# Performance work log

Measured on AMD Instinct MI355X. Metric: run time of the kernel, lower is better.

The kernel has to match this reference:

```python
import jax, jax.numpy as jnp
import numpy as np

B, S, F, H = 8, 2048, 512, 4
W = 32            # local window size
DH = F // H       # head dim
EPS = 1e-5


def layer_norm(x, w, b):
    mu = jnp.mean(x, axis=-1, keepdims=True)
    var = jnp.var(x, axis=-1, keepdims=True)
    return (x - mu) * jax.lax.rsqrt(var + EPS) * w + b


def mha(x, w_in, b_in, w_out, b_out):
    # x: [..., L, F]; torch nn.MultiheadAttention self-attention (dropout inactive / eval)
    qkv = x @ w_in.T + b_in                      # [..., L, 3F]
    q, k, v = jnp.split(qkv, 3, axis=-1)
    lead = x.shape[:-2]
    L = x.shape[-2]

    def heads(t):  # [..., L, F] -> [..., H, L, DH]
        return jnp.swapaxes(t.reshape(*lead, L, H, DH), -3, -2)

    q, k, v = heads(q), heads(k), heads(v)
    scores = jnp.einsum('...hld,...hmd->...hlm', q, k) / np.sqrt(DH)
    p = jax.nn.softmax(scores, axis=-1)
    o = jnp.einsum('...hlm,...hmd->...hld', p, v)  # [..., H, L, DH]
    o = jnp.swapaxes(o, -3, -2).reshape(*lead, L, F)
    return o @ w_out.T + b_out


def setup_inputs() -> dict:
    key = jax.random.key(0)
    ks = jax.random.split(key, 16)
    s = 0.02
    p = lambda k, shape: jax.random.normal(k, shape, dtype=jnp.float32) * s
    return {
        'x': jax.random.normal(ks[0], (B, S, F), dtype=jnp.float32),
        'l_in_w': p(ks[1], (3 * F, F)), 'l_in_b': p(ks[2], (3 * F,)),
        'l_out_w': p(ks[3], (F, F)),   'l_out_b': p(ks[4], (F,)),
        'g_in_w': p(ks[5], (3 * F, F)), 'g_in_b': p(ks[6], (3 * F,)),
        'g_out_w': p(ks[7], (F, F)),   'g_out_b': p(ks[8], (F,)),
        'n1_w': jnp.ones((F,)), 'n1_b': jnp.zeros((F,)),
        'n2_w': jnp.ones((F,)), 'n2_b': jnp.zeros((F,)),
        'gate_w': p(ks[9], (F, 2 * F)), 'gate_b': p(ks[10], (F,)),
        'gln_w': jnp.ones((F,)), 'gln_b': jnp.zeros((F,)),
    }


def reference(x, l_in_w, l_in_b, l_out_w, l_out_b,
              g_in_w, g_in_b, g_out_w, g_out_b,
              n1_w, n1_b, n2_w, n2_b,
              gate_w, gate_b, gln_w, gln_b):
    # local branch: block-diagonal (windowed) self-attention, all windows batched
    xw = x.reshape(B, S // W, W, F)
    local = mha(xw, l_in_w, l_in_b, l_out_w, l_out_b).reshape(B, S, F)
    local = layer_norm(x + local, n1_w, n1_b)
    # global branch: full self-attention
    glob = mha(x, g_in_w, g_in_b, g_out_w, g_out_b)
    glob = layer_norm(x + glob, n2_w, n2_b)
    # learned gate fusion
    gi = jnp.concatenate([local, glob], axis=-1)
    gate = jax.nn.sigmoid(layer_norm(gi @ gate_w.T + gate_b, gln_w, gln_b))
    return gate * local + (1.0 - gate) * glob
```

## Files before the change

### kernel.cpp

```cpp
#include <hip/hip_runtime.h>
#include <stdint.h>

#define BB 8
#define SS 2048
#define FF 512
#define HH 4
#define TOK (BB * SS)

typedef unsigned short u16;
typedef short short8 __attribute__((ext_vector_type(8)));
typedef float f32x4 __attribute__((ext_vector_type(4)));
typedef float f32x16 __attribute__((ext_vector_type(16)));

static __device__ __forceinline__ u16 f2bf(float f) {
  uint32_t u = __builtin_bit_cast(uint32_t, f);
  u = (u + 0x7fffu + ((u >> 16) & 1u)) >> 16;
  return (u16)u;
}

static __device__ __forceinline__ void cp16(void* lds, const void* g) {
  __builtin_amdgcn_global_load_lds(
      (const __attribute__((address_space(1))) void*)g,
      (__attribute__((address_space(3))) void*)lds, 16, 0, 0);
}

__global__ __launch_bounds__(256) void castk(const float* __restrict__ s,
                                             u16* __restrict__ d, int n) {
  const int i = (blockIdx.x * 256 + threadIdx.x) * 8;
  if (i >= n) return;
  float4 a = *(const float4*)(s + i);
  float4 b = *(const float4*)(s + i + 4);
  short8 o;
  o[0] = (short)f2bf(a.x); o[1] = (short)f2bf(a.y);
  o[2] = (short)f2bf(a.z); o[3] = (short)f2bf(a.w);
  o[4] = (short)f2bf(b.x); o[5] = (short)f2bf(b.y);
  o[6] = (short)f2bf(b.z); o[7] = (short)f2bf(b.w);
  *(short8*)(d + i) = o;
}

__global__ __launch_bounds__(256) void gemm_bt(
    const u16* __restrict__ A, const u16* __restrict__ B,
    const float* __restrict__ bias, float* __restrict__ Cf,
    u16* __restrict__ Cb, int M, int N, int K) {
  const int m0 = blockIdx.x << 7;
  const int n0 = blockIdx.y << 7;
  __shared__ u16 As[128 * 64];
  __shared__ u16 Bs[128 * 64];
  const int tid = threadIdx.x;
  const int wave = tid >> 6, lane = tid & 63;
  const int wr = wave >> 1, wc = wave & 1;

  f32x4 acc[4][4];
#pragma unroll
  for (int i = 0; i < 4; ++i)
#pragma unroll
    for (int j = 0; j < 4; ++j)
#pragma unroll
      for (int e = 0; e < 4; ++e) acc[i][j][e] = 0.f;

  for (int k0 = 0; k0 < K; k0 += 64) {
#pragma unroll
    for (int i = 0; i < 4; ++i) {
      const int base = (i * 4 + wave) << 10;
      const int lb = base + (lane << 4);
      const int r = lb >> 7;
      const int s = ((lb >> 4) & 7) ^ (r & 7);
      cp16((char*)As + base, A + (size_t)(m0 + r) * K + k0 + s * 8);
      cp16((char*)Bs + base, B + (size_t)(n0 + r) * K + k0 + s * 8);
    }
    __syncthreads();
#pragma unroll
    for (int kk = 0; kk < 2; ++kk) {
      short8 af[4], bfr[4];
#pragma unroll
      for (int mi = 0; mi < 4; ++mi) {
        const int r = wr * 64 + mi * 16 + (lane & 15);
        const int p = (kk * 4 + (lane >> 4)) ^ (r & 7);
        af[mi] = *(const short8*)(As + r * 64 + p * 8);
      }
#pragma unroll
      for (int ni = 0; ni < 4; ++ni) {
        const int r = wc * 64 + ni * 16 + (lane & 15);
        const int p = (kk * 4 + (lane >> 4)) ^ (r & 7);
        bfr[ni] = *(const short8*)(Bs + r * 64 + p * 8);
      }
#pragma unroll
      for (int mi = 0; mi < 4; ++mi)
#pragma unroll
        for (int ni = 0; ni < 4; ++ni)
          acc[mi][ni] = __builtin_amdgcn_mfma_f32_16x16x32_bf16(
              af[mi], bfr[ni], acc[mi][ni], 0, 0, 0);
    }
    __syncthreads();
  }
  const int rv = (lane >> 4) << 2;
  const int cn = lane & 15;
#pragma unroll
  for (int mi = 0; mi < 4; ++mi)
#pragma unroll
    for (int ni = 0; ni < 4; ++ni) {
      const int gn = n0 + wc * 64 + ni * 16 + cn;
      const float bv = bias ? bias[gn] : 0.f;
#pragma unroll
      for (int v = 0; v < 4; ++v) {
        const int gm = m0 + wr * 64 + mi * 16 + rv + v;
        const size_t off = (size_t)gm * N + gn;
        const float val = acc[mi][ni][v] + bv;
        if (Cf) Cf[off] = val;
        if (Cb) Cb[off] = f2bf(val);
      }
    }
}

__global__ __launch_bounds__(256) void transpose_v(
    const u16* __restrict__ qkv, u16* __restrict__ vt) {
  const int bh = blockIdx.x, st = blockIdx.y, dt = blockIdx.z;
  const int b = bh >> 2, h = bh & 3;
  __shared__ u16 t[64][72];
  const int r = threadIdx.x >> 3;
  const int c8 = (threadIdx.x & 7) * 8;
#pragma unroll
  for (int ph = 0; ph < 2; ++ph) {
    const int srow = ph * 32 + r;
    const u16* src = qkv + (size_t)(b * SS + st * 64 + srow) * 1536 + 1024 +
                     h * 128 + dt * 64 + c8;
    *(short8*)&t[srow][c8] = *(const short8*)src;
  }
  __syncthreads();
#pragma unroll
  for (int ph = 0; ph < 2; ++ph) {
    const int drow = ph * 32 + r;
    short8 o;
#pragma unroll
    for (int j = 0; j < 8; ++j) o[j] = (short)t[c8 + j][drow];
    *(short8*)(vt + ((size_t)bh * 128 + dt * 64 + drow) * SS + st * 64 + c8) = o;
  }
}

__global__ __launch_bounds__(256) void attn_local(
    const u16* __restrict__ qkv, const u16* __restrict__ vt,
    u16* __restrict__ ao) {
  const int wave = threadIdx.x >> 6, lane = threadIdx.x & 63;
  const int u = blockIdx.x * 4 + wave;
  const int b = u >> 8, w = (u >> 2) & 63, h = u & 3;
  const int q = lane & 31, half = lane >> 5;
  __shared__ u16 P[4][32][40];

  const size_t qbase = (size_t)(b * SS + w * 32 + q) * 1536 + h * 128;
  short8 qf[8];
#pragma unroll
  for (int d8 = 0; d8 < 8; ++d8)
    qf[d8] = *(const short8*)(qkv + qbase + d8 * 16 + half * 8);

  f32x16 s;
#pragma unroll
  for (int e = 0; e < 16; ++e) s[e] = 0.f;
  const size_t kbase = qbase + 512;
#pragma unroll
  for (int d8 = 0; d8 < 8; ++d8) {
    short8 kf = *(const short8*)(qkv + kbase + d8 * 16 + half * 8);
    s = __builtin_amdgcn_mfma_f32_32x32x16_bf16(kf, qf[d8], s, 0, 0, 0);
  }
  const float c1 = 0.12752725f;
  float m = -3e38f, t[16];
#pragma unroll
  for (int e = 0; e < 16; ++e) { t[e] = s[e] * c1; m = fmaxf(m, t[e]); }
  m = fmaxf(m, __shfl_xor(m, 32));
  float l = 0.f, p[16];
#pragma unroll
  for (int e = 0; e < 16; ++e) { p[e] = exp2f(t[e] - m); l += p[e]; }
  l += __shfl_xor(l, 32);
#pragma unroll
  for (int rr = 0; rr < 8; ++rr) {
    const int r0 = rr * 2;
    const int k0 = (r0 & 3) + 8 * (r0 >> 2) + 4 * half;
    uint32_t pk = (uint32_t)f2bf(p[r0]) | ((uint32_t)f2bf(p[r0 + 1]) << 16);
    *(uint32_t*)&P[wave][q][k0] = pk;
  }
  __syncthreads();
  f32x16 o[4];
#pragma unroll
  for (int nt = 0; nt < 4; ++nt)
#pragma unroll
    for (int e = 0; e < 16; ++e) o[nt][e] = 0.f;
  const size_t vbase = ((size_t)(b * 4 + h) * 128) * SS + w * 32;
#pragma unroll
  for (int ks = 0; ks < 2; ++ks) {
    short8 pa = *(const short8*)&P[wave][q][ks * 16 + half * 8];
#pragma unroll
    for (int nt = 0; nt < 4; ++nt) {
      short8 vb = *(const short8*)(vt + vbase + (size_t)(nt * 32 + q) * SS +
                                   ks * 16 + half * 8);
      o[nt] = __builtin_amdgcn_mfma_f32_32x32x16_bf16(pa, vb, o[nt], 0, 0, 0);
    }
  }
  const float rl = 1.f / l;
  const size_t ob = (size_t)(b * SS + w * 32) * FF + h * 128;
#pragma unroll
  for (int e = 0; e < 16; ++e) {
    const int qr = (e & 3) + 8 * (e >> 2) + 4 * half;
    const float rf = __shfl(rl, qr);
#pragma unroll
    for (int nt = 0; nt < 4; ++nt)
      ao[ob + (size_t)qr * FF + nt * 32 + q] = f2bf(o[nt][e] * rf);
  }
}

__global__ __launch_bounds__(256) void attn_global(
    const u16* __restrict__ qkv, const u16* __restrict__ vt,
    u16* __restrict__ ao) {
  const int lb = (blockIdx.x & 7) * 64 + (blockIdx.x >> 3);
  const int bh = lb >> 4, qt = lb & 15;
  const int b = bh >> 2, h = bh & 3;
  const int wave = threadIdx.x >> 6, lane = threadIdx.x & 63;
  const int q = lane & 31, half = lane >> 5;

  __shared__ u16 Ks[64 * 128];
  __shared__ u16 Vs[128 * 64];
  __shared__ u16 P[4][32][72];

  short8 qf[8];
  const size_t qb = (size_t)(b * SS + qt * 128 + wave * 32 + q) * 1536 + h * 128;
#pragma unroll
  for (int d8 = 0; d8 < 8; ++d8)
    qf[d8] = *(const short8*)(qkv + qb + d8 * 16 + half * 8);

  f32x16 o[4];
#pragma unroll
  for (int nt = 0; nt < 4; ++nt)
#pragma unroll
    for (int e = 0; e < 16; ++e) o[nt][e] = 0.f;
  float m = -3e38f, lsum = 0.f;
  const float c1 = 0.12752725f;

  const size_t kbase = (size_t)b * SS * 1536 + 512 + h * 128;
  const size_t vbase = (size_t)bh * 128 * SS;

  auto STAGE = [&](int kt) {
#pragma unroll
    for (int i = 0; i < 4; ++i) {
      const int base = (i * 4 + wave) << 10;
      const int lbk = base + (lane << 4);
      {
        const int r = lbk >> 8;
        const int sl = ((lbk >> 4) & 15) ^ (r & 7);
        cp16((char*)Ks + base,
             qkv + kbase + (size_t)(kt * 64 + r) * 1536 + sl * 8);
      }
      {
        const int d = lbk >> 7;
        const int sl = ((lbk >> 4) & 7) ^ (d & 7);
        cp16((char*)Vs + base, vt + vbase + (size_t)d * SS + kt * 64 + sl * 8);
      }
    }
  };
  STAGE(0);
  for (int kt = 0; kt < 32; ++kt) {
    __syncthreads();
    f32x16 sa[2];
#pragma unroll
    for (int mt = 0; mt < 2; ++mt)
#pragma unroll
      for (int e = 0; e < 16; ++e) sa[mt][e] = 0.f;
#pragma unroll
    for (int mt = 0; mt < 2; ++mt) {
      const int kr = mt * 32 + q;
#pragma unroll
      for (int d8 = 0; d8 < 8; ++d8) {
        const int ps = (d8 * 2 + half) ^ (kr & 7);
        short8 kf = *(const short8*)(Ks + kr * 128 + ps * 8);
        sa[mt] = __builtin_amdgcn_mfma_f32_32x32x16_bf16(kf, qf[d8], sa[mt], 0, 0, 0);
      }
    }
    float tv[32];
    float mn = m;
#pragma unroll
    for (int e = 0; e < 16; ++e) { tv[e] = sa[0][e] * c1; tv[16 + e] = sa[1][e] * c1; }
#pragma unroll
    for (int e = 0; e < 32; ++e) mn = fmaxf(mn, tv[e]);
    mn = fmaxf(mn, __shfl_xor(mn, 32));
    const float corr = exp2f(m - mn);
    m = mn;
    float la = 0.f;
#pragma unroll
    for (int e = 0; e < 32; ++e) { tv[e] = exp2f(tv[e] - mn); la += tv[e]; }
    la += __shfl_xor(la, 32);
    lsum = lsum * corr + la;
#pragma unroll
    for (int e = 0; e < 16; ++e) {
      const float cf = __shfl(corr, (e & 3) + 8 * (e >> 2) + 4 * half);
#pragma unroll
      for (int nt = 0; nt < 4; ++nt) o[nt][e] *= cf;
    }
#pragma unroll
    for (int mt = 0; mt < 2; ++mt)
#pragma unroll
      for (int rr = 0; rr < 8; ++rr) {
        const int r0 = rr * 2;
        const int k0 = (r0 & 3) + 8 * (r0 >> 2) + 4 * half + mt * 32;
        uint32_t pk = (uint32_t)f2bf(tv[mt * 16 + r0]) |
                      ((uint32_t)f2bf(tv[mt * 16 + r0 + 1]) << 16);
        *(uint32_t*)&P[wave][q][k0] = pk;
      }
    __syncthreads();
#pragma unroll
    for (int ks = 0; ks < 4; ++ks) {
      short8 pa = *(const short8*)&P[wave][q][ks * 16 + half * 8];
#pragma unroll
      for (int nt = 0; nt < 4; ++nt) {
        const int d = nt * 32 + q;
        const int ps = (ks * 2 + half) ^ (d & 7);
        short8 vb = *(const short8*)(Vs + d * 64 + ps * 8);
        o[nt] = __builtin_amdgcn_mfma_f32_32x32x16_bf16(pa, vb, o[nt], 0, 0, 0);
      }
    }
    __syncthreads();
    if (kt + 1 < 32) STAGE(kt + 1);
  }
  const float rl = 1.f / lsum;
  const size_t ob = (size_t)(b * SS + qt * 128 + wave * 32) * FF + h * 128;
#pragma unroll
  for (int e = 0; e < 16; ++e) {
    const int qr = (e & 3) + 8 * (e >> 2) + 4 * half;
    const float rf = __shfl(rl, qr);
#pragma unroll
    for (int nt = 0; nt < 4; ++nt)
      ao[ob + (size_t)qr * FF + nt * 32 + q] = f2bf(o[nt][e] * rf);
  }
}

__global__ __launch_bounds__(256) void resid_ln(
    float* __restrict__ y, const float* __restrict__ x,
    const float* __restrict__ w, const float* __restrict__ bv_,
    u16* __restrict__ lg) {
  const int wave = threadIdx.x >> 6, lane = threadIdx.x & 63;
  const size_t row = (size_t)blockIdx.x * 4 + wave;
  const int c = lane * 8;
  float* yr = y + row * FF;
  const float* xr = x + row * FF;
  float v[8];
  {
    float4 a0 = *(const float4*)(yr + c), a1 = *(const float4*)(yr + c + 4);
    float4 b0 = *(const float4*)(xr + c), b1 = *(const float4*)(xr + c + 4);
    v[0] = a0.x + b0.x; v[1] = a0.y + b0.y; v[2] = a0.z + b0.z; v[3] = a0.w + b0.w;
    v[4] = a1.x + b1.x; v[5] = a1.y + b1.y; v[6] = a1.z + b1.z; v[7] = a1.w + b1.w;
  }
  float s = 0.f, s2 = 0.f;
#pragma unroll
  for (int e = 0; e < 8; ++e) { s += v[e]; s2 += v[e] * v[e]; }
#pragma unroll
  for (int off = 1; off < 64; off <<= 1) {
    s += __shfl_xor(s, off);
    s2 += __shfl_xor(s2, off);
  }
  const float mu = s * (1.f / 512.f);
  const float var = s2 * (1.f / 512.f) - mu * mu;
  const float rs = rsqrtf(var + 1e-5f);
  float4 w0 = *(const float4*)(w + c), w1 = *(const float4*)(w + c + 4);
  float4 b0 = *(const float4*)(bv_ + c), b1 = *(const float4*)(bv_ + c + 4);
  const float wv[8] = {w0.x, w0.y, w0.z, w0.w, w1.x, w1.y, w1.z, w1.w};
  const float bb[8] = {b0.x, b0.y, b0.z, b0.w, b1.x, b1.y, b1.z, b1.w};
  short8 ob;
#pragma unroll
  for (int e = 0; e < 8; ++e) {
    v[e] = (v[e] - mu) * rs * wv[e] + bb[e];
    ob[e] = (short)f2bf(v[e]);
  }
  *(float4*)(yr + c) = make_float4(v[0], v[1], v[2], v[3]);
  *(float4*)(yr + c + 4) = make_float4(v[4], v[5], v[6], v[7]);
  *(short8*)(lg + row * 1024 + c) = ob;
}

__global__ __launch_bounds__(256) void gate_final(
    const float* __restrict__ gp, const float* __restrict__ loc,
    const float* __restrict__ glo, const float* __restrict__ w,
    const float* __restrict__ bv_, float* __restrict__ out) {
  const int wave = threadIdx.x >> 6, lane = threadIdx.x & 63;
  const size_t row = (size_t)blockIdx.x * 4 + wave;
  const int c = lane * 8;
  const float* gr = gp + row * FF;
  float v[8];
  {
    float4 a0 = *(const float4*)(gr + c), a1 = *(const float4*)(gr + c + 4);
    v[0] = a0.x; v[1] = a0.y; v[2] = a0.z; v[3] = a0.w;
    v[4] = a1.x; v[5] = a1.y; v[6] = a1.z; v[7] = a1.w;
  }
  float s = 0.f, s2 = 0.f;
#pragma unroll
  for (int e = 0; e < 8; ++e) { s += v[e]; s2 += v[e] * v[e]; }
#pragma unroll
  for (int off = 1; off < 64; off <<= 1) {
    s += __shfl_xor(s, off);
    s2 += __shfl_xor(s2, off);
  }
  const float mu = s * (1.f / 512.f);
  const float var = s2 * (1.f / 512.f) - mu * mu;
  const float rs = rsqrtf(var + 1e-5f);
  float4 w0 = *(const float4*)(w + c), w1 = *(const float4*)(w + c + 4);
  float4 b0 = *(const float4*)(bv_ + c), b1 = *(const float4*)(bv_ + c + 4);
  const float wv[8] = {w0.x, w0.y, w0.z, w0.w, w1.x, w1.y, w1.z, w1.w};
  const float bb[8] = {b0.x, b0.y, b0.z, b0.w, b1.x, b1.y, b1.z, b1.w};
  float4 l0 = *(const float4*)(loc + row * FF + c), l1 = *(const float4*)(loc + row * FF + c + 4);
  float4 g0 = *(const float4*)(glo + row * FF + c), g1 = *(const float4*)(glo + row * FF + c + 4);
  const float lv[8] = {l0.x, l0.y, l0.z, l0.w, l1.x, l1.y, l1.z, l1.w};
  const float gv[8] = {g0.x, g0.y, g0.z, g0.w, g1.x, g1.y, g1.z, g1.w};
  float r[8];
#pragma unroll
  for (int e = 0; e < 8; ++e) {
    const float z = (v[e] - mu) * rs * wv[e] + bb[e];
    const float gt = 1.f / (1.f + exp2f(-1.44269504f * z));
    r[e] = gt * lv[e] + (1.f - gt) * gv[e];
  }
  *(float4*)(out + row * FF + c) = make_float4(r[0], r[1], r[2], r[3]);
  *(float4*)(out + row * FF + c + 4) = make_float4(r[4], r[5], r[6], r[7]);
}

extern "C" void kernel_launch(void* const* d_in, const int* in_sizes, int n_in,
                              void* d_out, int out_size, void* d_ws,
                              size_t ws_size, hipStream_t stream) {
  const float* x       = (const float*)d_in[0];
  const float* l_in_w  = (const float*)d_in[1];
  const float* l_in_b  = (const float*)d_in[2];
  const float* l_out_w = (const float*)d_in[3];
  const float* l_out_b = (const float*)d_in[4];
  const float* g_in_w  = (const float*)d_in[5];
  const float* g_in_b  = (const float*)d_in[6];
  const float* g_out_w = (const float*)d_in[7];
  const float* g_out_b = (const float*)d_in[8];
  const float* n1_w    = (const float*)d_in[9];
  const float* n1_b    = (const float*)d_in[10];
  const float* n2_w    = (const float*)d_in[11];
  const float* n2_b    = (const float*)d_in[12];
  const float* gate_w  = (const float*)d_in[13];
  const float* gate_b  = (const float*)d_in[14];
  const float* gln_w   = (const float*)d_in[15];
  const float* gln_b   = (const float*)d_in[16];
  float* out = (float*)d_out;

  char* ws = (char*)d_ws;
  u16* x_bf  = (u16*)(ws);
  u16* w_liw = (u16*)(ws + 16777216);
  u16* w_giw = (u16*)(ws + 18350080);
  u16* w_low = (u16*)(ws + 19922944);
  u16* w_gow = (u16*)(ws + 20447232);
  u16* w_gt  = (u16*)(ws + 20971520);
  u16* qkv   = (u16*)(ws + 22020096);
  u16* vt    = (u16*)(ws + 72351744);
  u16* ato   = (u16*)(ws + 89128960);
  float* locf = (float*)(ws + 105906176);
  float* glof = (float*)(ws + 139460608);
  u16* lgbf  = (u16*)(ws + 173015040);
  float* gpre = (float*)(ws + 22020096);

  castk<<<4096, 256, 0, stream>>>(x, x_bf, 8388608);
  castk<<<384, 256, 0, stream>>>(l_in_w, w_liw, 786432);
  castk<<<384, 256, 0, stream>>>(g_in_w, w_giw, 786432);
  castk<<<128, 256, 0, stream>>>(l_out_w, w_low, 262144);
  castk<<<128, 256, 0, stream>>>(g_out_w, w_gow, 262144);
  castk<<<256, 256, 0, stream>>>(gate_w, w_gt, 524288);

  gemm_bt<<<dim3(128, 12), 256, 0, stream>>>(x_bf, w_liw, l_in_b, nullptr, qkv,
                                             TOK, 1536, 512);
  transpose_v<<<dim3(32, 32, 2), 256, 0, stream>>>(qkv, vt);
  attn_local<<<512, 256, 0, stream>>>(qkv, vt, ato);
  gemm_bt<<<dim3(128, 4), 256, 0, stream>>>(ato, w_low, l_out_b, locf, nullptr,
                                            TOK, 512, 512);
  resid_ln<<<4096, 256, 0, stream>>>(locf, x, n1_w, n1_b, lgbf);

  gemm_bt<<<dim3(128, 12), 256, 0, stream>>>(x_bf, w_giw, g_in_b, nullptr, qkv,
                                             TOK, 1536, 512);
  transpose_v<<<dim3(32, 32, 2), 256, 0, stream>>>(qkv, vt);
  attn_global<<<512, 256, 0, stream>>>(qkv, vt, ato);
  gemm_bt<<<dim3(128, 4), 256, 0, stream>>>(ato, w_gow, g_out_b, glof, nullptr,
                                            TOK, 512, 512);
  resid_ln<<<4096, 256, 0, stream>>>(glof, x, n2_w, n2_b, lgbf + 512);

  gemm_bt<<<dim3(128, 4), 256, 0, stream>>>(lgbf, w_gt, gate_b, gpre, nullptr,
                                            TOK, 512, 1024);
  gate_final<<<4096, 256, 0, stream>>>(gpre, locf, glof, gln_w, gln_b, out);
}
```

Baseline: 528.5 us.

## Keep softmax P in registers, double-buffer K/V, fold scale into QKV GEMM

Folds the softmax scale (1/sqrt(DH)·log2e) into the Q columns of the QKV projection epilogue, so the attention kernels no longer multiply scores. Both attention kernels now build the P operand in registers with packed bf16 conversion and permlane32 swaps, removing the LDS round-trip and a barrier per tile. The global attention double-buffers K/V tiles so the next tile's loads overlap compute, and it applies a lazy max rescale that only corrects the accumulators when the running max grows by more than a threshold. The costs are more LDS for the second buffer, which may lower occupancy, and the lazy rescale, which leaves up to a 2^8 factor in exponentials and so adds some precision risk.

```diff
diff --git a/kernel.cpp b/kernel.cpp
--- a/kernel.cpp
+++ b/kernel.cpp
@@ -11,11 +11,18 @@
 typedef short short8 __attribute__((ext_vector_type(8)));
 typedef float f32x4 __attribute__((ext_vector_type(4)));
 typedef float f32x16 __attribute__((ext_vector_type(16)));
+typedef unsigned int u32x4 __attribute__((ext_vector_type(4)));
 
 static __device__ __forceinline__ u16 f2bf(float f) {
   uint32_t u = __builtin_bit_cast(uint32_t, f);
   u = (u + 0x7fffu + ((u >> 16) & 1u)) >> 16;
   return (u16)u;
+}
+
+static __device__ __forceinline__ uint32_t cvtpk(float lo, float hi) {
+  uint32_t r;
+  asm("v_cvt_pk_bf16_f32 %0, %1, %2" : "=v"(r) : "v"(lo), "v"(hi));
+  return r;
 }
 
 static __device__ __forceinline__ void cp16(void* lds, const void* g) {
@@ -41,7 +48,7 @@
 __global__ __launch_bounds__(256) void gemm_bt(
     const u16* __restrict__ A, const u16* __restrict__ B,
     const float* __restrict__ bias, float* __restrict__ Cf,
-    u16* __restrict__ Cb, int M, int N, int K) {
+    u16* __restrict__ Cb, int M, int N, int K, int qcols, float qscale) {
   const int m0 = blockIdx.x << 7;
   const int n0 = blockIdx.y << 7;
   __shared__ u16 As[128 * 64];
@@ -101,11 +108,12 @@
     for (int ni = 0; ni < 4; ++ni) {
       const int gn = n0 + wc * 64 + ni * 16 + cn;
       const float bv = bias ? bias[gn] : 0.f;
+      const float sc = (gn < qcols) ? qscale : 1.f;
 #pragma unroll
       for (int v = 0; v < 4; ++v) {
         const int gm = m0 + wr * 64 + mi * 16 + rv + v;
         const size_t off = (size_t)gm * N + gn;
-        const float val = acc[mi][ni][v] + bv;
+        const float val = (acc[mi][ni][v] + bv) * sc;
         if (Cf) Cf[off] = val;
         if (Cb) Cb[off] = f2bf(val);
       }
@@ -137,6 +145,21 @@
   }
 }
 
+template <typename GET>
+static __device__ __forceinline__ short8 make_pa(int ks, GET get) {
+  const int c0 = (2 * ks) & 3;
+  u32x4 pw;
+#pragma unroll
+  for (int t = 0; t < 2; ++t) {
+    uint32_t a = cvtpk(get(4 * c0 + 2 * t), get(4 * c0 + 2 * t + 1));
+    uint32_t b = cvtpk(get(4 * (c0 + 1) + 2 * t), get(4 * (c0 + 1) + 2 * t + 1));
+    auto r = __builtin_amdgcn_permlane32_swap(a, b, false, false);
+    pw[t] = r[0];
+    pw[2 + t] = r[1];
+  }
+  return __builtin_bit_cast(short8, pw);
+}
+
 __global__ __launch_bounds__(256) void attn_local(
     const u16* __restrict__ qkv, const u16* __restrict__ vt,
     u16* __restrict__ ao) {
@@ -144,7 +167,6 @@
   const int u = blockIdx.x * 4 + wave;
   const int b = u >> 8, w = (u >> 2) & 63, h = u & 3;
   const int q = lane & 31, half = lane >> 5;
-  __shared__ u16 P[4][32][40];
 
   const size_t qbase = (size_t)(b * SS + w * 32 + q) * 1536 + h * 128;
   short8 qf[8];
@@ -161,23 +183,15 @@
     short8 kf = *(const short8*)(qkv + kbase + d8 * 16 + half * 8);
     s = __builtin_amdgcn_mfma_f32_32x32x16_bf16(kf, qf[d8], s, 0, 0, 0);
   }
-  const float c1 = 0.12752725f;
-  float m = -3e38f, t[16];
-#pragma unroll
-  for (int e = 0; e < 16; ++e) { t[e] = s[e] * c1; m = fmaxf(m, t[e]); }
+  float m = s[0];
+#pragma unroll
+  for (int e = 1; e < 16; ++e) m = fmaxf(m, s[e]);
   m = fmaxf(m, __shfl_xor(m, 32));
-  float l = 0.f, p[16];
-#pragma unroll
-  for (int e = 0; e < 16; ++e) { p[e] = exp2f(t[e] - m); l += p[e]; }
+  float l = 0.f;
+#pragma unroll
+  for (int e = 0; e < 16; ++e) { s[e] = exp2f(s[e] - m); l += s[e]; }
   l += __shfl_xor(l, 32);
-#pragma unroll
-  for (int rr = 0; rr < 8; ++rr) {
-    const int r0 = rr * 2;
-    const int k0 = (r0 & 3) + 8 * (r0 >> 2) + 4 * half;
-    uint32_t pk = (uint32_t)f2bf(p[r0]) | ((uint32_t)f2bf(p[r0 + 1]) << 16);
-    *(uint32_t*)&P[wave][q][k0] = pk;
-  }
-  __syncthreads();
+
   f32x16 o[4];
 #pragma unroll
   for (int nt = 0; nt < 4; ++nt)
@@ -186,7 +200,7 @@
   const size_t vbase = ((size_t)(b * 4 + h) * 128) * SS + w * 32;
 #pragma unroll
   for (int ks = 0; ks < 2; ++ks) {
-    short8 pa = *(const short8*)&P[wave][q][ks * 16 + half * 8];
+    short8 pa = make_pa(ks, [&](int e) { return s[e]; });
 #pragma unroll
     for (int nt = 0; nt < 4; ++nt) {
       short8 vb = *(const short8*)(vt + vbase + (size_t)(nt * 32 + q) * SS +
@@ -215,9 +229,8 @@
   const int wave = threadIdx.x >> 6, lane = threadIdx.x & 63;
   const int q = lane & 31, half = lane >> 5;
 
-  __shared__ u16 Ks[64 * 128];
-  __shared__ u16 Vs[128 * 64];
-  __shared__ u16 P[4][32][72];
+  __shared__ u16 Ks[2][64 * 128];
+  __shared__ u16 Vs[2][128 * 64];
 
   short8 qf[8];
   const size_t qb = (size_t)(b * SS + qt * 128 + wave * 32 + q) * 1536 + h * 128;
@@ -231,12 +244,13 @@
 #pragma unroll
     for (int e = 0; e < 16; ++e) o[nt][e] = 0.f;
   float m = -3e38f, lsum = 0.f;
-  const float c1 = 0.12752725f;
 
   const size_t kbase = (size_t)b * SS * 1536 + 512 + h * 128;
   const size_t vbase = (size_t)bh * 128 * SS;
 
-  auto STAGE = [&](int kt) {
+  auto STAGE = [&](int kt, int bsel) {
+    u16* kd = Ks[bsel];
+    u16* vd = Vs[bsel];
 #pragma unroll
     for (int i = 0; i < 4; ++i) {
       const int base = (i * 4 + wave) << 10;
@@ -244,19 +258,24 @@
       {
         const int r = lbk >> 8;
         const int sl = ((lbk >> 4) & 15) ^ (r & 7);
-        cp16((char*)Ks + base,
+        cp16((char*)kd + base,
              qkv + kbase + (size_t)(kt * 64 + r) * 1536 + sl * 8);
       }
       {
         const int d = lbk >> 7;
         const int sl = ((lbk >> 4) & 7) ^ (d & 7);
-        cp16((char*)Vs + base, vt + vbase + (size_t)d * SS + kt * 64 + sl * 8);
+        cp16((char*)vd + base, vt + vbase + (size_t)d * SS + kt * 64 + sl * 8);
       }
     }
   };
-  STAGE(0);
+  STAGE(0, 0);
+  __syncthreads();
   for (int kt = 0; kt < 32; ++kt) {
-    __syncthreads();
+    const int cur = kt & 1;
+    if (kt + 1 < 32) STAGE(kt + 1, cur ^ 1);
+    const u16* Kb = Ks[cur];
+    const u16* Vb = Vs[cur];
+
     f32x16 sa[2];
 #pragma unroll
     for (int mt = 0; mt < 2; ++mt)
@@ -268,54 +287,51 @@
 #pragma unroll
       for (int d8 = 0; d8 < 8; ++d8) {
         const int ps = (d8 * 2 + half) ^ (kr & 7);
-        short8 kf = *(const short8*)(Ks + kr * 128 + ps * 8);
+        short8 kf = *(const short8*)(Kb + kr * 128 + ps * 8);
         sa[mt] = __builtin_amdgcn_mfma_f32_32x32x16_bf16(kf, qf[d8], sa[mt], 0, 0, 0);
       }
     }
-    float tv[32];
-    float mn = m;
-#pragma unroll
-    for (int e = 0; e < 16; ++e) { tv[e] = sa[0][e] * c1; tv[16 + e] = sa[1][e] * c1; }
-#pragma unroll
-    for (int e = 0; e < 32; ++e) mn = fmaxf(mn, tv[e]);
-    mn = fmaxf(mn, __shfl_xor(mn, 32));
-    const float corr = exp2f(m - mn);
-    m = mn;
+    float pmax = sa[0][0];
+#pragma unroll
+    for (int e = 1; e < 16; ++e) pmax = fmaxf(pmax, sa[0][e]);
+#pragma unroll
+    for (int e = 0; e < 16; ++e) pmax = fmaxf(pmax, sa[1][e]);
+    pmax = fmaxf(pmax, __shfl_xor(pmax, 32));
+    if (__any(pmax > m + 8.f)) {
+      const float mn = fmaxf(m, pmax);
+      const float corr = exp2f(m - mn);
+      m = mn;
+      lsum *= corr;
+#pragma unroll
+      for (int e = 0; e < 16; ++e) {
+        const float cf = __shfl(corr, (e & 3) + 8 * (e >> 2) + 4 * half);
+#pragma unroll
+        for (int nt = 0; nt < 4; ++nt) o[nt][e] *= cf;
+      }
+    }
     float la = 0.f;
 #pragma unroll
-    for (int e = 0; e < 32; ++e) { tv[e] = exp2f(tv[e] - mn); la += tv[e]; }
+    for (int mt = 0; mt < 2; ++mt)
+#pragma unroll
+      for (int e = 0; e < 16; ++e) {
+        sa[mt][e] = exp2f(sa[mt][e] - m);
+        la += sa[mt][e];
+      }
     la += __shfl_xor(la, 32);
-    lsum = lsum * corr + la;
-#pragma unroll
-    for (int e = 0; e < 16; ++e) {
-      const float cf = __shfl(corr, (e & 3) + 8 * (e >> 2) + 4 * half);
-#pragma unroll
-      for (int nt = 0; nt < 4; ++nt) o[nt][e] *= cf;
-    }
-#pragma unroll
-    for (int mt = 0; mt < 2; ++mt)
-#pragma unroll
-      for (int rr = 0; rr < 8; ++rr) {
-        const int r0 = rr * 2;
-        const int k0 = (r0 & 3) + 8 * (r0 >> 2) + 4 * half + mt * 32;
-        uint32_t pk = (uint32_t)f2bf(tv[mt * 16 + r0]) |
-                      ((uint32_t)f2bf(tv[mt * 16 + r0 + 1]) << 16);
-        *(uint32_t*)&P[wave][q][k0] = pk;
-      }
-    __syncthreads();
+    lsum += la;
 #pragma unroll
     for (int ks = 0; ks < 4; ++ks) {
-      short8 pa = *(const short8*)&P[wave][q][ks * 16 + half * 8];
+      const int mt = ks >> 1;
+      short8 pa = make_pa(ks, [&](int e) { return sa[mt][e]; });
 #pragma unroll
       for (int nt = 0; nt < 4; ++nt) {
         const int d = nt * 32 + q;
         const int ps = (ks * 2 + half) ^ (d & 7);
-        short8 vb = *(const short8*)(Vs + d * 64 + ps * 8);
+        short8 vb = *(const short8*)(Vb + d * 64 + ps * 8);
         o[nt] = __builtin_amdgcn_mfma_f32_32x32x16_bf16(pa, vb, o[nt], 0, 0, 0);
       }
     }
     __syncthreads();
-    if (kt + 1 < 32) STAGE(kt + 1);
   }
   const float rl = 1.f / lsum;
   const size_t ob = (size_t)(b * SS + qt * 128 + wave * 32) * FF + h * 128;
@@ -437,6 +453,8 @@
   const float* gln_b   = (const float*)d_in[16];
   float* out = (float*)d_out;
 
+  const float c1 = 0.12752724808f;
+
   char* ws = (char*)d_ws;
   u16* x_bf  = (u16*)(ws);
   u16* w_liw = (u16*)(ws + 16777216);
@@ -460,22 +478,22 @@
   castk<<<256, 256, 0, stream>>>(gate_w, w_gt, 524288);
 
   gemm_bt<<<dim3(128, 12), 256, 0, stream>>>(x_bf, w_liw, l_in_b, nullptr, qkv,
-                                             TOK, 1536, 512);
+                                             TOK, 1536, 512, 512, c1);
   transpose_v<<<dim3(32, 32, 2), 256, 0, stream>>>(qkv, vt);
   attn_local<<<512, 256, 0, stream>>>(qkv, vt, ato);
   gemm_bt<<<dim3(128, 4), 256, 0, stream>>>(ato, w_low, l_out_b, locf, nullptr,
-                                            TOK, 512, 512);
+                                            TOK, 512, 512, 0, 1.f);
   resid_ln<<<4096, 256, 0, stream>>>(locf, x, n1_w, n1_b, lgbf);
 
   gemm_bt<<<dim3(128, 12), 256, 0, stream>>>(x_bf, w_giw, g_in_b, nullptr, qkv,
-                                             TOK, 1536, 512);
+                                             TOK, 1536, 512, 512, c1);
   transpose_v<<<dim3(32, 32, 2), 256, 0, stream>>>(qkv, vt);
   attn_global<<<512, 256, 0, stream>>>(qkv, vt, ato);
   gemm_bt<<<dim3(128, 4), 256, 0, stream>>>(ato, w_gow, g_out_b, glof, nullptr,
-                                            TOK, 512, 512);
+                                            TOK, 512, 512, 0, 1.f);
   resid_ln<<<4096, 256, 0, stream>>>(glof, x, n2_w, n2_b, lgbf + 512);
 
   gemm_bt<<<dim3(128, 4), 256, 0, stream>>>(lgbf, w_gt, gate_b, gpre, nullptr,
-                                            TOK, 512, 1024);
+                                            TOK, 512, 1024, 0, 1.f);
   gate_final<<<4096, 256, 0, stream>>>(gpre, locf, glof, gln_w, gln_b, out);
 }
```

After: 471.6 us. 10.8% less time.
